# Kernel tuning notes

Hardware: AMD Instinct MI355X
Metric: run time of the kernel (lower is better)

The kernel has to match this reference:

```python
import jax, jax.numpy as jnp
import numpy as np

EPS = 1e-06


def _make_spd(key, b, d, dtype=jnp.float32):
    x = jax.random.normal(key, (b, d, d), dtype=dtype)
    # X X^T / d + 0.5 I  -> well-conditioned SPD
    return jnp.matmul(x, jnp.swapaxes(x, -1, -2)) / d + 0.5 * jnp.eye(d, dtype=dtype)


def setup_inputs() -> dict:
    key = jax.random.key(0)
    k1, k2, k3 = jax.random.split(key, 3)
    B, D, E = 8192, 64, 32
    return {
        "recon_x": _make_spd(k1, B, D),
        "orig_x": _make_spd(k2, B, D),
        "encoded_x": _make_spd(k3, B, E),
    }


def _sqrt_det(mats):
    # faithful to torch.potrf(A).diag().prod(): product of Cholesky diagonal
    # (i.e. sqrt(det(A))), batched over leading dim.
    L = jnp.linalg.cholesky(mats)  # [B, D, D]
    diag = jnp.diagonal(L, axis1=-2, axis2=-1)  # [B, D]
    return jnp.prod(diag, axis=-1)  # [B]


def _batched_trace(mats):
    return jnp.trace(mats, axis1=-2, axis2=-1)


def reference(recon_x, orig_x, encoded_x):
    dim = orig_x.shape[-1]
    # KL(A || B) = 0.5 * (tr(B^{-1} A) - dim + log((sdetA+eps)/(sdetB+eps)))
    sdet_A = _sqrt_det(orig_x) + EPS
    sdet_B = _sqrt_det(recon_x) + EPS
    logdet = jnp.log(sdet_A / sdet_B)
    tr = _batched_trace(jnp.linalg.solve(recon_x, orig_x))  # tr(B^{-1} A), batched
    kl_rec = 0.5 * (tr - dim + logdet)  # [B]
    kl_loss_reconstruction = -jnp.sum(kl_rec)

    # KL(encoded || I): B = I => B^{-1}A = A, sqrt(det(I)) = 1
    e_dim = encoded_x.shape[-1]
    sdet_E = _sqrt_det(encoded_x) + EPS
    logdet_e = jnp.log(sdet_E / (1.0 + EPS))
    tr_e = _batched_trace(encoded_x)
    kl_enc = 0.5 * (tr_e - e_dim + logdet_e)  # [B]
    kl_loss_encoding = -jnp.sum(kl_enc)

    loss = kl_loss_encoding + kl_loss_reconstruction
    return (loss, kl_loss_reconstruction, kl_loss_encoding)
```

## Files before the change

### kernel.cpp

```cpp
#include <hip/hip_runtime.h>
#include <math.h>

#define EPS 1e-6f

__device__ __forceinline__ float bcast(float x, int srcLane) {
    return __int_as_float(__builtin_amdgcn_readlane(__float_as_int(x), srcLane));
}

__global__ __launch_bounds__(256, 1) void vae_rec_kernel(const float* __restrict__ recon,
                                                         const float* __restrict__ orig,
                                                         float* __restrict__ out,
                                                         int npairs) {
    const int lane = threadIdx.x & 63;
    const int waveInBlock = threadIdx.x >> 6;
    const int pair = blockIdx.x * 4 + waveInBlock;

    float kl = 0.0f;
    if (pair < npairs) {
        const float* Bm = recon + (size_t)pair * 4096;
        const float* Am = orig + (size_t)pair * 4096;

        float rB[64], rA[64];
        {
            const float4* pb = (const float4*)(Bm + lane * 64);
            const float4* pa = (const float4*)(Am + lane * 64);
#pragma unroll
            for (int i = 0; i < 16; ++i) {
                float4 vb = pb[i];
                float4 va = pa[i];
                rB[4 * i + 0] = vb.x; rB[4 * i + 1] = vb.y;
                rB[4 * i + 2] = vb.z; rB[4 * i + 3] = vb.w;
                rA[4 * i + 0] = va.x; rA[4 * i + 1] = va.y;
                rA[4 * i + 2] = va.z; rA[4 * i + 3] = va.w;
            }
        }

        float detB = 1.0f, detA = 1.0f;
#pragma unroll
        for (int k = 0; k < 64; ++k) {
            float bkk = bcast(rB[k], k);
            float akk = bcast(rA[k], k);
            detB *= bkk;
            detA *= akk;
            float ib = __builtin_amdgcn_rsqf(bkk);
            float ia = __builtin_amdgcn_rsqf(akk);
            rB[k] *= ib;
            rA[k] *= ia;
#pragma unroll
            for (int j = k + 1; j < 64; ++j) {
                float lbj = bcast(rB[k], j);
                float laj = bcast(rA[k], j);
                rB[j] = __builtin_fmaf(-rB[k], lbj, rB[j]);
                rA[j] = __builtin_fmaf(-rA[k], laj, rA[j]);
            }
        }

        float fro = 0.0f;
#pragma unroll
        for (int i = 0; i < 64; ++i) {
            float bii = bcast(rB[i], i);
            float inv = __builtin_amdgcn_rcpf(bii);
            float t = rB[i] * inv;
            float acc = 0.0f;
#pragma unroll
            for (int c = 0; c <= i; ++c) {
                float u = bcast(rA[c], i);
                acc = __builtin_fmaf(u, u, acc);
                rA[c] = __builtin_fmaf(-t, u, rA[c]);
            }
            fro = __builtin_fmaf(acc, inv * inv, fro);
        }

        float sdetB = __builtin_sqrtf(detB);
        float sdetA = __builtin_sqrtf(detA);
        float logdet = __builtin_logf((sdetA + EPS) / (sdetB + EPS));
        kl = 0.5f * (fro - 64.0f + logdet);
    }

    __shared__ float sred[4];
    if (lane == 0) sred[waveInBlock] = kl;
    __syncthreads();
    if (threadIdx.x == 0) {
        float s = sred[0] + sred[1] + sred[2] + sred[3];
        atomicAdd(out + 1, -s);
    }
}

__global__ __launch_bounds__(256, 1) void vae_enc_kernel(const float* __restrict__ enc,
                                                         float* __restrict__ out,
                                                         int nmats) {
    const int lane = threadIdx.x & 63;
    const int r = lane & 31;
    const bool hi = lane >= 32;
    const int wv = (int)(blockIdx.x * 4 + (threadIdx.x >> 6));
    const int mat = wv * 2 + (hi ? 1 : 0);

    float kl = 0.0f;
    if (mat < nmats) {
        const float* M = enc + (size_t)mat * 1024;
        float rm[32];
        {
            const float4* pm = (const float4*)(M + r * 32);
#pragma unroll
            for (int i = 0; i < 8; ++i) {
                float4 v = pm[i];
                rm[4 * i + 0] = v.x; rm[4 * i + 1] = v.y;
                rm[4 * i + 2] = v.z; rm[4 * i + 3] = v.w;
            }
        }

        float tr = 0.0f;
#pragma unroll
        for (int i = 0; i < 32; ++i)
            if (i == r) tr = rm[i];
#pragma unroll
        for (int m = 1; m < 32; m <<= 1)
            tr += __shfl_xor(tr, m, 64);

        float det = 1.0f;
#pragma unroll
        for (int k = 0; k < 32; ++k) {
            float a0 = bcast(rm[k], k);
            float a1 = bcast(rm[k], k + 32);
            float akk = hi ? a1 : a0;
            det *= akk;
            float inv = __builtin_amdgcn_rsqf(akk);
            rm[k] *= inv;
#pragma unroll
            for (int j = k + 1; j < 32; ++j) {
                float l0 = bcast(rm[k], j);
                float l1 = bcast(rm[k], j + 32);
                float ljk = hi ? l1 : l0;
                rm[j] = __builtin_fmaf(-rm[k], ljk, rm[j]);
            }
        }

        float sdet = __builtin_sqrtf(det);
        float logdet = __builtin_logf((sdet + EPS) / (1.0f + EPS));
        kl = 0.5f * (tr - 32.0f + logdet);
    }

    __shared__ float sred[8];
    if (r == 0) sred[threadIdx.x >> 5] = kl;
    __syncthreads();
    if (threadIdx.x == 0) {
        float s = 0.0f;
#pragma unroll
        for (int i = 0; i < 8; ++i) s += sred[i];
        atomicAdd(out + 2, -s);
    }
}

__global__ void vae_init_kernel(float* __restrict__ out) {
    if (threadIdx.x < 3) out[threadIdx.x] = 0.0f;
}

__global__ void vae_final_kernel(float* __restrict__ out) {
    if (threadIdx.x == 0) out[0] = out[1] + out[2];
}

extern "C" void kernel_launch(void* const* d_in, const int* in_sizes, int n_in,
                              void* d_out, int out_size, void* d_ws, size_t ws_size,
                              hipStream_t stream) {
    const float* recon = (const float*)d_in[0];
    const float* orig = (const float*)d_in[1];
    const float* enc = (const float*)d_in[2];
    float* out = (float*)d_out;

    const int npairs = in_sizes[0] / 4096;
    const int nmats = in_sizes[2] / 1024;

    vae_init_kernel<<<1, 64, 0, stream>>>(out);

    const int rec_blocks = (npairs + 3) / 4;
    vae_rec_kernel<<<rec_blocks, 256, 0, stream>>>(recon, orig, out, npairs);

    const int enc_blocks = (nmats + 7) / 8;
    vae_enc_kernel<<<enc_blocks, 256, 0, stream>>>(enc, out, nmats);

    vae_final_kernel<<<1, 64, 0, stream>>>(out);
}
```

Before: 476.0 us.

## Serialize Cholesky of B then fuse A's Cholesky with the triangular solve

The reconstruction kernel now factors B alone first, then loads A and interleaves A's Cholesky step k with the forward-substitution/Frobenius step k. This keeps only one 64-float matrix live during the first phase, and launch bounds are raised to 2 blocks per CU to allow more occupancy. The aim is to cut register pressure so more waves can hide latency. The cost is that A's load is no longer overlapped with B's factorization, and the column-k update of rA during the solve must stay valid for the rows A's Cholesky has not finished yet.

Measured after the change: 1.032 ms. 2.17x slower.

```diff
diff --git a/kernel.cpp b/kernel.cpp
--- a/kernel.cpp
+++ b/kernel.cpp
@@ -7,7 +7,7 @@
     return __int_as_float(__builtin_amdgcn_readlane(__float_as_int(x), srcLane));
 }
 
-__global__ __launch_bounds__(256, 1) void vae_rec_kernel(const float* __restrict__ recon,
+__global__ __launch_bounds__(256, 2) void vae_rec_kernel(const float* __restrict__ recon,
                                                          const float* __restrict__ orig,
                                                          float* __restrict__ out,
                                                          int npairs) {
@@ -20,53 +20,63 @@
         const float* Bm = recon + (size_t)pair * 4096;
         const float* Am = orig + (size_t)pair * 4096;
 
-        float rB[64], rA[64];
+        float rB[64];
         {
             const float4* pb = (const float4*)(Bm + lane * 64);
+#pragma unroll
+            for (int i = 0; i < 16; ++i) {
+                float4 v = pb[i];
+                rB[4 * i + 0] = v.x; rB[4 * i + 1] = v.y;
+                rB[4 * i + 2] = v.z; rB[4 * i + 3] = v.w;
+            }
+        }
+        float detB = 1.0f;
+#pragma unroll
+        for (int k = 0; k < 64; ++k) {
+            float bkk = bcast(rB[k], k);
+            detB *= bkk;
+            float ib = __builtin_amdgcn_rsqf(bkk);
+            rB[k] *= ib;
+#pragma unroll
+            for (int j = k + 1; j < 64; ++j) {
+                float c = bcast(rB[k], j);
+                rB[j] = __builtin_fmaf(-rB[k], c, rB[j]);
+            }
+        }
+
+        __builtin_amdgcn_sched_barrier(0);
+
+        float rA[64];
+        {
             const float4* pa = (const float4*)(Am + lane * 64);
 #pragma unroll
             for (int i = 0; i < 16; ++i) {
-                float4 vb = pb[i];
-                float4 va = pa[i];
-                rB[4 * i + 0] = vb.x; rB[4 * i + 1] = vb.y;
-                rB[4 * i + 2] = vb.z; rB[4 * i + 3] = vb.w;
-                rA[4 * i + 0] = va.x; rA[4 * i + 1] = va.y;
-                rA[4 * i + 2] = va.z; rA[4 * i + 3] = va.w;
+                float4 v = pa[i];
+                rA[4 * i + 0] = v.x; rA[4 * i + 1] = v.y;
+                rA[4 * i + 2] = v.z; rA[4 * i + 3] = v.w;
             }
         }
-
-        float detB = 1.0f, detA = 1.0f;
+        float detA = 1.0f, fro = 0.0f;
 #pragma unroll
         for (int k = 0; k < 64; ++k) {
-            float bkk = bcast(rB[k], k);
             float akk = bcast(rA[k], k);
-            detB *= bkk;
             detA *= akk;
-            float ib = __builtin_amdgcn_rsqf(bkk);
             float ia = __builtin_amdgcn_rsqf(akk);
-            rB[k] *= ib;
             rA[k] *= ia;
 #pragma unroll
             for (int j = k + 1; j < 64; ++j) {
-                float lbj = bcast(rB[k], j);
-                float laj = bcast(rA[k], j);
-                rB[j] = __builtin_fmaf(-rB[k], lbj, rB[j]);
-                rA[j] = __builtin_fmaf(-rA[k], laj, rA[j]);
+                float c = bcast(rA[k], j);
+                rA[j] = __builtin_fmaf(-rA[k], c, rA[j]);
             }
-        }
-
-        float fro = 0.0f;
-#pragma unroll
-        for (int i = 0; i < 64; ++i) {
-            float bii = bcast(rB[i], i);
+            float bii = bcast(rB[k], k);
             float inv = __builtin_amdgcn_rcpf(bii);
-            float t = rB[i] * inv;
+            float t = rB[k] * inv;
             float acc = 0.0f;
 #pragma unroll
-            for (int c = 0; c <= i; ++c) {
-                float u = bcast(rA[c], i);
+            for (int c2 = 0; c2 <= k; ++c2) {
+                float u = bcast(rA[c2], k);
                 acc = __builtin_fmaf(u, u, acc);
-                rA[c] = __builtin_fmaf(-t, u, rA[c]);
+                rA[c2] = __builtin_fmaf(-t, u, rA[c2]);
             }
             fro = __builtin_fmaf(acc, inv * inv, fro);
         }
```
